# Kernel tuning notes

Hardware: AMD Instinct MI355X
Metric: run time of the kernel (lower is better)

The kernel has to match this reference:

```python
import jax, jax.numpy as jnp
import numpy as np

N = 50000          # nodes
E = 1600000        # edges (avg degree 32)
G = 16             # graphs in batch
H = 128            # hidden_dim
HOP = 3
IN_DIM = 1


def setup_inputs() -> dict:
    key = jax.random.key(0)
    ks = jax.random.split(key, 12)
    s = 1.0 / np.sqrt(H)
    return {
        "x": jax.random.normal(ks[0], (N, IN_DIM), jnp.float32),
        "edge_index": jax.random.randint(ks[1], (2, E), 0, N, jnp.int64),
        "edge_attr": jax.random.uniform(ks[2], (E, 1), jnp.float32),
        "batch": jnp.sort(jax.random.randint(ks[3], (N,), 0, G, jnp.int64)),
        "W1": jax.random.normal(ks[4], (HOP, H, IN_DIM), jnp.float32) * s,
        "W2": jax.random.normal(ks[5], (HOP, H, H), jnp.float32) * s,
        "W3": jax.random.normal(ks[6], (HOP, H, H), jnp.float32) * s,
        "W4": jax.random.normal(ks[7], (HOP, H, 1), jnp.float32) * s,
        "W5": jax.random.normal(ks[8], (1, 2 * H), jnp.float32) * s,
        "b5": jnp.zeros((1,), jnp.float32),
        "W6": jax.random.normal(ks[9], (H, H), jnp.float32) * s,
        "W7": jax.random.normal(ks[10], (H, H), jnp.float32) * s,
    }


def reference(x, edge_index, edge_attr, batch, W1, W2, W3, W4, W5, b5, W6, W7):
    row, col = edge_index[0], edge_index[1]
    node_emb = jnp.zeros((N, H), x.dtype)
    for l in range(HOP):
        nfe = x @ W1[l].T                                        # [N,H]
        # gather neighbor embeddings along col, scatter-add to row
        ne_aggr = jax.ops.segment_sum(node_emb[col], row, num_segments=N)
        efe = jax.nn.relu(edge_attr @ W4[l].T)                   # [E,H]
        ee_aggr = jax.ops.segment_sum(efe, row, num_segments=N)  # [N,H]
        node_emb = jax.nn.relu(nfe + ne_aggr @ W2[l].T + ee_aggr @ W3[l].T)
    pooled = jax.ops.segment_sum(node_emb, batch, num_segments=G)  # [G,H]
    sum_emb = pooled @ W6.T                                        # [G,H]
    cat = jax.nn.relu(jnp.concatenate([sum_emb[batch], node_emb @ W7.T], axis=-1))
    return cat @ W5.T + b5                                         # [N,1]
```

## Files before the change

### kernel.cpp

```cpp
#include <hip/hip_runtime.h>
#include <hip/hip_bf16.h>

#define N_NODES 50000
#define N_EDGES 1600000
#define NGRAPH  16
#define HID     128

#define RPB   128
#define NB    ((N_NODES + RPB - 1) / RPB)
#define NBLK  256
#define EPB   ((N_EDGES + NBLK - 1) / NBLK)
#define P4CAP 6144

typedef unsigned int uint32;
typedef unsigned short ushort;
typedef unsigned char uchar;
typedef __attribute__((ext_vector_type(8))) short bf16x8;
typedef __attribute__((ext_vector_type(4))) float f32x4;
typedef __attribute__((ext_vector_type(2))) float f32x2;

__device__ __forceinline__ uint32 bf16r(float f) {
    uint32 b = __float_as_uint(f);
    return (b + 0x7fffu + ((b >> 16) & 1u)) >> 16;
}
__device__ __forceinline__ uint32 pack_bf16(float lo, float hi) {
    return bf16r(lo) | (bf16r(hi) << 16);
}

__global__ __launch_bounds__(256) void k_init(float* __restrict__ zp, int nz,
                                              const float* __restrict__ W2,
                                              const float* __restrict__ W7,
                                              const float* __restrict__ W3,
                                              const float* __restrict__ W4,
                                              ushort* __restrict__ wpack,
                                              float* __restrict__ v3) {
    int idx = blockIdx.x * 256 + threadIdx.x;
    if (idx < nz) zp[idx] = 0.f;
    if (idx < 4 * 16384) {
        int m = idx >> 14, f = idx & 16383;
        int j = f & 7, lane = (f >> 3) & 63, kk = (f >> 9) & 3, t = (f >> 11) & 7;
        int hp = t * 16 + (lane & 15);
        int k  = kk * 32 + ((lane >> 4) & 3) * 8 + j;
        const float* src = (m < 3) ? (W2 + m * HID * HID) : W7;
        wpack[idx] = (ushort)bf16r(src[hp * HID + k]);
    }
    if (idx < 3 * HID) {
        int l = idx / HID, hp = idx % HID;
        float acc = 0.f;
        for (int h = 0; h < HID; h++)
            acc += W3[l * HID * HID + hp * HID + h] * fmaxf(W4[l * HID + h], 0.f);
        v3[idx] = acc;
    }
}

__global__ __launch_bounds__(1024) void k_p1_hist(const int* __restrict__ row,
                                                  int* __restrict__ blkhist) {
    __shared__ int hist[NB];
    int tid = threadIdx.x, blk = blockIdx.x;
    for (int i = tid; i < NB; i += 1024) hist[i] = 0;
    __syncthreads();
    int s = blk * EPB, e = s + EPB; if (e > N_EDGES) e = N_EDGES;
    for (int i = s + tid; i < e; i += 1024)
        atomicAdd(&hist[row[i] >> 7], 1);
    __syncthreads();
    for (int i = tid; i < NB; i += 1024)
        blkhist[i * NBLK + blk] = hist[i];
}

__global__ __launch_bounds__(NBLK) void k_p2a(int* __restrict__ blkhist,
                                              int* __restrict__ btot) {
    __shared__ int sums[NBLK];
    int t = threadIdx.x, b = blockIdx.x;
    int v = blkhist[b * NBLK + t];
    sums[t] = v;
    __syncthreads();
    for (int d = 1; d < NBLK; d <<= 1) {
        int u = (t >= d) ? sums[t - d] : 0;
        __syncthreads();
        sums[t] += u;
        __syncthreads();
    }
    blkhist[b * NBLK + t] = sums[t] - v;
    if (t == NBLK - 1) btot[b] = sums[t];
}

__global__ __launch_bounds__(1024) void k_p3_part(const int* __restrict__ row,
                                                  const int* __restrict__ col,
                                                  const float* __restrict__ ea,
                                                  const int* __restrict__ blkhist,
                                                  const int* __restrict__ btot,
                                                  int2* __restrict__ pea) {
    __shared__ int sc[512];
    __shared__ int cur[NB];
    int tid = threadIdx.x, blk = blockIdx.x;
    if (tid < 512) sc[tid] = (tid < NB) ? btot[tid] : 0;
    __syncthreads();
    for (int d = 1; d < 512; d <<= 1) {
        int v = 0;
        if (tid < 512 && tid >= d) v = sc[tid - d];
        __syncthreads();
        if (tid < 512) sc[tid] += v;
        __syncthreads();
    }
    for (int i = tid; i < NB; i += 1024)
        cur[i] = (sc[i] - btot[i]) + blkhist[i * NBLK + blk];
    __syncthreads();
    int s = blk * EPB, e = s + EPB; if (e > N_EDGES) e = N_EDGES;
    for (int i = s + tid; i < e; i += 1024) {
        int r = row[i], c = col[i];
        float a = ea[i];
        int slot = atomicAdd(&cur[r >> 7], 1);
        pea[slot] = make_int2(((r & (RPB - 1)) << 16) | c, __float_as_int(a));
    }
}

__global__ __launch_bounds__(512) void k_p4(const int2* __restrict__ pea,
                                            const int* __restrict__ btot,
                                            const float* __restrict__ x,
                                            int* __restrict__ offs,
                                            float* __restrict__ ea_sum,
                                            int* __restrict__ csr,
                                            uchar* __restrict__ emb0,
                                            const float* __restrict__ w1l0,
                                            const float* __restrict__ v3l0) {
    __shared__ int2  cache[P4CAP];
    __shared__ int   red[512];
    __shared__ int   cnt[RPB];
    __shared__ float eas[RPB];
    __shared__ int   scan_s[RPB];
    __shared__ int   curp[RPB];
    int t = threadIdx.x, b = blockIdx.x;
    red[t] = (t < b) ? btot[t] : 0;
    __syncthreads();
    for (int d = 256; d > 0; d >>= 1) {
        if (t < d) red[t] += red[t + d];
        __syncthreads();
    }
    int s = red[0];
    int e = s + btot[b];
    int len = e - s;
    int clen = len < P4CAP ? len : P4CAP;
    for (int i = t; i < clen; i += 512) cache[i] = pea[s + i];
    if (t < RPB) { cnt[t] = 0; eas[t] = 0.f; }
    __syncthreads();
    for (int i = t; i < len; i += 512) {
        int2 p = (i < P4CAP) ? cache[i] : pea[s + i];
        int lr = ((uint32)p.x) >> 16;
        atomicAdd(&cnt[lr], 1);
        atomicAdd(&eas[lr], __int_as_float(p.y));
    }
    __syncthreads();
    if (t < RPB) scan_s[t] = cnt[t];
    __syncthreads();
    for (int d = 1; d < RPB; d <<= 1) {
        int v = 0;
        if (t < RPB && t >= d) v = scan_s[t - d];
        __syncthreads();
        if (t < RPB) scan_s[t] += v;
        __syncthreads();
    }
    int nbase = b * RPB;
    if (t < RPB) {
        int excl = scan_s[t] - cnt[t];
        int n = nbase + t;
        if (n < N_NODES) {
            offs[n] = s + excl;
            ea_sum[n] = eas[t];
        }
        curp[t] = s + excl;
    }
    if (b == NB - 1 && t == 0) offs[N_NODES] = e;
    __syncthreads();
    for (int i = t; i < len; i += 512) {
        int2 p = (i < P4CAP) ? cache[i] : pea[s + i];
        int slot = atomicAdd(&curp[((uint32)p.x) >> 16], 1);
        csr[slot] = p.x & 0xFFFF;
    }
    for (int i = t; i < RPB * 32; i += 512) {
        int lr = i >> 5, c4 = (i & 31) * 4;
        int n = nbase + lr;
        if (n < N_NODES) {
            float xv = x[n];
            float ev = eas[lr];
            float v0 = fmaxf(xv * w1l0[c4 + 0] + ev * v3l0[c4 + 0], 0.f) * 0.015625f;
            float v1 = fmaxf(xv * w1l0[c4 + 1] + ev * v3l0[c4 + 1], 0.f) * 0.015625f;
            float v2 = fmaxf(xv * w1l0[c4 + 2] + ev * v3l0[c4 + 2], 0.f) * 0.015625f;
            float v3v = fmaxf(xv * w1l0[c4 + 3] + ev * v3l0[c4 + 3], 0.f) * 0.015625f;
            int u = __builtin_amdgcn_cvt_pk_fp8_f32(v0, v1, 0, false);
            u = __builtin_amdgcn_cvt_pk_fp8_f32(v2, v3v, u, true);
            *(uint32*)(emb0 + (size_t)n * 128 + c4) = (uint32)u;
        }
    }
}

__global__ __launch_bounds__(256) void k_gather(const uchar* __restrict__ emb,
                                                const int* __restrict__ offs,
                                                const int* __restrict__ csr,
                                                uint32* __restrict__ agg) {
    int node = (blockIdx.x * 256 + threadIdx.x) >> 6;
    int lane = threadIdx.x & 63;
    if (node >= N_NODES) return;
    int s = offs[node], e = offs[node + 1];
    int off2 = 2 * lane;
    float ax[8] = {0.f}, ay[8] = {0.f};
    for (int base = s; base < e; base += 64) {
        int idx = base + lane;
        int cv = (idx < e) ? csr[idx] : 0;
        int cnt = e - base; if (cnt > 64) cnt = 64;
        int j = 0;
        for (; j + 16 <= cnt; j += 16) {
            int h16[16];
#pragma unroll
            for (int u = 0; u < 16; u++) {
                uint32 c = (uint32)__builtin_amdgcn_readlane(cv, j + u);
                h16[u] = *(const ushort*)(emb + (((size_t)c) << 7) + off2);
            }
#pragma unroll
            for (int u = 0; u < 16; u++) {
                f32x2 d = __builtin_amdgcn_cvt_pk_f32_fp8(h16[u], false);
                ax[u & 7] += d.x; ay[u & 7] += d.y;
            }
        }
        for (; j + 4 <= cnt; j += 4) {
            int h4[4];
#pragma unroll
            for (int u = 0; u < 4; u++) {
                uint32 c = (uint32)__builtin_amdgcn_readlane(cv, j + u);
                h4[u] = *(const ushort*)(emb + (((size_t)c) << 7) + off2);
            }
#pragma unroll
            for (int u = 0; u < 4; u++) {
                f32x2 d = __builtin_amdgcn_cvt_pk_f32_fp8(h4[u], false);
                ax[u] += d.x; ay[u] += d.y;
            }
        }
        for (; j < cnt; j++) {
            uint32 c = (uint32)__builtin_amdgcn_readlane(cv, j);
            int h = *(const ushort*)(emb + (((size_t)c) << 7) + off2);
            f32x2 d = __builtin_amdgcn_cvt_pk_f32_fp8(h, false);
            ax[0] += d.x; ay[0] += d.y;
        }
    }
    float rx = (((ax[0] + ax[1]) + (ax[2] + ax[3])) + ((ax[4] + ax[5]) + (ax[6] + ax[7]))) * 64.f;
    float ry = (((ay[0] + ay[1]) + (ay[2] + ay[3])) + ((ay[4] + ay[5]) + (ay[6] + ay[7]))) * 64.f;
    agg[(size_t)node * 64 + lane] = pack_bf16(rx, ry);
}

#define LROW 136

template <bool LAST>
__global__ __launch_bounds__(256) void k_gemm(const uint32* __restrict__ agg,
                                              const ushort* __restrict__ w2p,
                                              const float* __restrict__ w1l,
                                              const float* __restrict__ v3l,
                                              const float* __restrict__ x,
                                              const float* __restrict__ ea_sum,
                                              uchar* __restrict__ emb8Out,
                                              const ushort* __restrict__ w7p,
                                              const float* __restrict__ W5,
                                              float* __restrict__ outp,
                                              const int* __restrict__ batch,
                                              float* __restrict__ pooled) {
    __shared__ ushort tile[64 * LROW];
    __shared__ float redp[4][128];
    int tid = threadIdx.x;
    int tbase = blockIdx.x * 64;
    int wv = tid >> 6, lane = tid & 63;
    int n0 = lane & 15, quad = lane >> 4;
    int arow = wv * 16 + n0;
    bf16x8 a0 = {0,0,0,0,0,0,0,0}, a1 = a0, a2 = a0, a3 = a0;
    if (tbase + arow < N_NODES) {
        const bf16x8* ap = (const bf16x8*)(agg + (size_t)(tbase + arow) * 64);
        a0 = ap[0 + quad]; a1 = ap[4 + quad]; a2 = ap[8 + quad]; a3 = ap[12 + quad];
    }
    const bf16x8* wb = (const bf16x8*)w2p;
    f32x4 acc[8];
#pragma unroll
    for (int t = 0; t < 8; t++) {
        f32x4 c = {0.f, 0.f, 0.f, 0.f};
        c = __builtin_amdgcn_mfma_f32_16x16x32_bf16(a0, wb[(t * 4 + 0) * 64 + lane], c, 0, 0, 0);
        c = __builtin_amdgcn_mfma_f32_16x16x32_bf16(a1, wb[(t * 4 + 1) * 64 + lane], c, 0, 0, 0);
        c = __builtin_amdgcn_mfma_f32_16x16x32_bf16(a2, wb[(t * 4 + 2) * 64 + lane], c, 0, 0, 0);
        c = __builtin_amdgcn_mfma_f32_16x16x32_bf16(a3, wb[(t * 4 + 3) * 64 + lane], c, 0, 0, 0);
        acc[t] = c;
    }
    float xs[4], es[4];
#pragma unroll
    for (int r = 0; r < 4; r++) {
        int n = tbase + wv * 16 + quad * 4 + r;
        xs[r] = (n < N_NODES) ? x[n] : 0.f;
        es[r] = (n < N_NODES) ? ea_sum[n] : 0.f;
    }
    if (!LAST) {
        uchar* stile = (uchar*)tile;
#pragma unroll
        for (int t = 0; t < 8; t++) {
            int hp = t * 16 + n0;
            float w1v = w1l[hp], v3v = v3l[hp];
#pragma unroll
            for (int r = 0; r < 4; r++) {
                float v = fmaxf(acc[t][r] + xs[r] * w1v + es[r] * v3v, 0.f) * 0.015625f;
                int enc = __builtin_amdgcn_cvt_pk_fp8_f32(v, v, 0, false);
                stile[(wv * 16 + quad * 4 + r) * 136 + hp] = (uchar)(enc & 0xff);
            }
        }
        __syncthreads();
        int vn = N_NODES - tbase; if (vn > 64) vn = 64;
        for (int i = tid; i < 64 * 32; i += 256) {
            int r = i >> 5, c4 = (i & 31) * 4;
            if (r < vn) {
                uint32 u = *(const uint32*)&stile[r * 136 + c4];
                *(uint32*)(emb8Out + (size_t)(tbase + r) * 128 + c4) = u;
            }
        }
    } else {
        int nlast = tbase + 63; if (nlast > N_NODES - 1) nlast = N_NODES - 1;
        int g0 = batch[tbase];
        bool uni = (batch[nlast] == g0);
        int gr[4];
        if (!uni) {
#pragma unroll
            for (int r = 0; r < 4; r++) {
                int n = tbase + wv * 16 + quad * 4 + r;
                gr[r] = (n < N_NODES) ? batch[n] : 0;
            }
        }
        float st[8];
#pragma unroll
        for (int t = 0; t < 8; t++) {
            int hp = t * 16 + n0;
            float w1v = w1l[hp], v3v = v3l[hp];
            float stt = 0.f;
#pragma unroll
            for (int r = 0; r < 4; r++) {
                float v = fmaxf(acc[t][r] + xs[r] * w1v + es[r] * v3v, 0.f);
                tile[(wv * 16 + quad * 4 + r) * LROW + hp] = (ushort)bf16r(v);
                if (uni) {
                    stt += v;
                } else {
                    int n = tbase + wv * 16 + quad * 4 + r;
                    if (n < N_NODES) atomicAdd(&pooled[gr[r] * HID + hp], v);
                }
            }
            st[t] = stt;
        }
        if (uni) {
#pragma unroll
            for (int t = 0; t < 8; t++) {
                float v = st[t];
                v += __shfl_xor(v, 16);
                v += __shfl_xor(v, 32);
                if (lane < 16) redp[wv][t * 16 + lane] = v;
            }
        }
        __syncthreads();
        if (uni && tid < 128) {
            float sp = (redp[0][tid] + redp[1][tid]) + (redp[2][tid] + redp[3][tid]);
            atomicAdd(&pooled[g0 * HID + tid], sp);
        }
        bf16x8 b0 = *(const bf16x8*)&tile[arow * LROW + 0 * 32 + quad * 8];
        bf16x8 b1 = *(const bf16x8*)&tile[arow * LROW + 1 * 32 + quad * 8];
        bf16x8 b2 = *(const bf16x8*)&tile[arow * LROW + 2 * 32 + quad * 8];
        bf16x8 b3 = *(const bf16x8*)&tile[arow * LROW + 3 * 32 + quad * 8];
        const bf16x8* w7 = (const bf16x8*)w7p;
        float p[4] = {0.f, 0.f, 0.f, 0.f};
#pragma unroll
        for (int t = 0; t < 8; t++) {
            f32x4 c = {0.f, 0.f, 0.f, 0.f};
            c = __builtin_amdgcn_mfma_f32_16x16x32_bf16(b0, w7[(t * 4 + 0) * 64 + lane], c, 0, 0, 0);
            c = __builtin_amdgcn_mfma_f32_16x16x32_bf16(b1, w7[(t * 4 + 1) * 64 + lane], c, 0, 0, 0);
            c = __builtin_amdgcn_mfma_f32_16x16x32_bf16(b2, w7[(t * 4 + 2) * 64 + lane], c, 0, 0, 0);
            c = __builtin_amdgcn_mfma_f32_16x16x32_bf16(b3, w7[(t * 4 + 3) * 64 + lane], c, 0, 0, 0);
            float w5v = W5[128 + t * 16 + n0];
#pragma unroll
            for (int r = 0; r < 4; r++) p[r] += fmaxf(c[r], 0.f) * w5v;
        }
#pragma unroll
        for (int r = 0; r < 4; r++) {
            float v = p[r];
            v += __shfl_xor(v, 1);
            v += __shfl_xor(v, 2);
            v += __shfl_xor(v, 4);
            v += __shfl_xor(v, 8);
            int n = tbase + wv * 16 + quad * 4 + r;
            if (n0 == 0 && n < N_NODES) outp[n] = v;
        }
    }
}

__global__ __launch_bounds__(256) void k_tail(float* __restrict__ out,
                                              const int* __restrict__ batch,
                                              const float* __restrict__ pooled,
                                              const float* __restrict__ W6,
                                              const float* __restrict__ W5,
                                              const float* __restrict__ b5) {
    __shared__ float red[256];
    __shared__ int gsh[2];
    int t = threadIdx.x;
    int nbase = blockIdx.x * 256;
    int n = nbase + t;
    if (t == 0) gsh[0] = batch[nbase < N_NODES ? nbase : N_NODES - 1];
    if (t == 1) gsh[1] = batch[(nbase + 255) < N_NODES ? (nbase + 255) : N_NODES - 1];
    __syncthreads();
    int g_lo = gsh[0], g_hi = gsh[1];
    int hp = t & 127;
    int g = (t >> 7) ? g_hi : g_lo;
    const float* pg = pooled + g * HID;
    const float* wr = W6 + hp * HID;
    float acc = 0.f;
    for (int h = 0; h < HID; h++) acc += pg[h] * wr[h];
    red[t] = fmaxf(acc, 0.f) * W5[hp];
    __syncthreads();
    for (int d = 64; d > 0; d >>= 1) {
        if (hp < d) red[t] += red[t + d];
        __syncthreads();
    }
    float s_lo = red[0], s_hi = red[128];
    if (n < N_NODES) {
        int gn = batch[n];
        float s;
        if (gn == g_lo) s = s_lo;
        else if (gn == g_hi) s = s_hi;
        else {
            s = 0.f;
            const float* pg2 = pooled + gn * HID;
            for (int hp2 = 0; hp2 < HID; hp2++) {
                float a2 = 0.f;
                for (int h = 0; h < HID; h++) a2 += pg2[h] * W6[hp2 * HID + h];
                s += fmaxf(a2, 0.f) * W5[hp2];
            }
        }
        out[n] += s + b5[0];
    }
}

extern "C" void kernel_launch(void* const* d_in, const int* in_sizes, int n_in,
                              void* d_out, int out_size, void* d_ws, size_t ws_size,
                              hipStream_t stream) {
    (void)in_sizes; (void)n_in; (void)out_size; (void)ws_size;
    const float* x    = (const float*)d_in[0];
    const int*   ei   = (const int*)d_in[1];
    const float* ea   = (const float*)d_in[2];
    const int*   bat  = (const int*)d_in[3];
    const float* W1   = (const float*)d_in[4];
    const float* W2   = (const float*)d_in[5];
    const float* W3   = (const float*)d_in[6];
    const float* W4   = (const float*)d_in[7];
    const float* W5   = (const float*)d_in[8];
    const float* b5   = (const float*)d_in[9];
    const float* W6   = (const float*)d_in[10];
    const float* W7   = (const float*)d_in[11];
    float* out = (float*)d_out;

    const int* row = ei;
    const int* col = ei + N_EDGES;

    float* wsf = (float*)d_ws;
    int*   wsi = (int*)d_ws;
    size_t o = 0;
    float* pooled = wsf + o; o += NGRAPH * HID;
    size_t ztot = o;
    int*   offs   = wsi + o; o += N_NODES + 1;
    float* ea_sum = wsf + o; o += N_NODES;
    int*   btot   = wsi + o; o += NB;
    float* v3     = wsf + o; o += 3 * HID;
    int*   blkh   = wsi + o; o += NB * NBLK;
    o = (o + 3) & ~(size_t)3;
    ushort* wpack = (ushort*)(wsi + o); o += 4 * 16384 / 2;
    int*    csr   = wsi + o; o += N_EDGES;
    o = (o + 1) & ~(size_t)1;
    int2*   pea   = (int2*)(wsi + o); o += 2 * (size_t)N_EDGES;
    uint32* aggB  = (uint32*)(wsi + o); o += (size_t)N_NODES * 64;
    uchar*  emb8  = (uchar*)(wsi + o);  o += (size_t)N_NODES * 32;
    uchar*  emb0  = (uchar*)(wsi + o);  o += (size_t)N_NODES * 32;

    const ushort* w2p1 = wpack + 1 * 16384;
    const ushort* w2p2 = wpack + 2 * 16384;
    const ushort* w7p  = wpack + 3 * 16384;

    k_init<<<(4 * 16384 + 255) / 256, 256, 0, stream>>>(
        (float*)d_ws, (int)ztot, W2, W7, W3, W4, (ushort*)wpack, v3);
    k_p1_hist<<<NBLK, 1024, 0, stream>>>(row, blkh);
    k_p2a<<<NB, NBLK, 0, stream>>>(blkh, btot);
    k_p3_part<<<NBLK, 1024, 0, stream>>>(row, col, ea, blkh, btot, pea);
    k_p4<<<NB, 512, 0, stream>>>(pea, btot, x, offs, ea_sum, csr, emb0, W1, v3);
    k_gather<<<(N_NODES * 64 + 255) / 256, 256, 0, stream>>>(emb0, offs, csr, aggB);
    k_gemm<false><<<(N_NODES + 63) / 64, 256, 0, stream>>>(
        aggB, w2p1, W1 + 1 * HID, v3 + 1 * HID, x, ea_sum, emb8, nullptr, nullptr, nullptr,
        nullptr, nullptr);
    k_gather<<<(N_NODES * 64 + 255) / 256, 256, 0, stream>>>(emb8, offs, csr, aggB);
    k_gemm<true><<<(N_NODES + 63) / 64, 256, 0, stream>>>(
        aggB, w2p2, W1 + 2 * HID, v3 + 2 * HID, x, ea_sum, nullptr, w7p, W5, out, bat, pooled);
    k_tail<<<(N_NODES + 255) / 256, 256, 0, stream>>>(out, bat, pooled, W6, W5, b5);
}
```

Baseline: 259.7 us.

## Fuse neighbor gather into per-hop GEMM kernel via shared-memory tile

The separate gather kernel and GEMM kernel are merged into one k_hop kernel. Each wave aggregates 16 nodes sequentially into a bf16 LDS tile, which the MFMA GEMM then reads directly. This removes the aggB global round trip and two kernel launches, and the next node's CSR indices are prefetched while the current one is processed. In exchange, parallelism per node drops from one wave per node to one wave per 16 nodes processed serially, which can lower memory-level parallelism for the latency-bound gather.

```diff
diff --git a/kernel.cpp b/kernel.cpp
--- a/kernel.cpp
+++ b/kernel.cpp
@@ -193,86 +193,104 @@
     }
 }
 
-__global__ __launch_bounds__(256) void k_gather(const uchar* __restrict__ emb,
-                                                const int* __restrict__ offs,
-                                                const int* __restrict__ csr,
-                                                uint32* __restrict__ agg) {
-    int node = (blockIdx.x * 256 + threadIdx.x) >> 6;
-    int lane = threadIdx.x & 63;
-    if (node >= N_NODES) return;
-    int s = offs[node], e = offs[node + 1];
-    int off2 = 2 * lane;
-    float ax[8] = {0.f}, ay[8] = {0.f};
-    for (int base = s; base < e; base += 64) {
-        int idx = base + lane;
-        int cv = (idx < e) ? csr[idx] : 0;
-        int cnt = e - base; if (cnt > 64) cnt = 64;
-        int j = 0;
-        for (; j + 16 <= cnt; j += 16) {
-            int h16[16];
-#pragma unroll
-            for (int u = 0; u < 16; u++) {
-                uint32 c = (uint32)__builtin_amdgcn_readlane(cv, j + u);
-                h16[u] = *(const ushort*)(emb + (((size_t)c) << 7) + off2);
-            }
-#pragma unroll
-            for (int u = 0; u < 16; u++) {
-                f32x2 d = __builtin_amdgcn_cvt_pk_f32_fp8(h16[u], false);
-                ax[u & 7] += d.x; ay[u & 7] += d.y;
-            }
-        }
-        for (; j + 4 <= cnt; j += 4) {
-            int h4[4];
-#pragma unroll
-            for (int u = 0; u < 4; u++) {
-                uint32 c = (uint32)__builtin_amdgcn_readlane(cv, j + u);
-                h4[u] = *(const ushort*)(emb + (((size_t)c) << 7) + off2);
-            }
-#pragma unroll
-            for (int u = 0; u < 4; u++) {
-                f32x2 d = __builtin_amdgcn_cvt_pk_f32_fp8(h4[u], false);
-                ax[u] += d.x; ay[u] += d.y;
-            }
-        }
-        for (; j < cnt; j++) {
-            uint32 c = (uint32)__builtin_amdgcn_readlane(cv, j);
-            int h = *(const ushort*)(emb + (((size_t)c) << 7) + off2);
-            f32x2 d = __builtin_amdgcn_cvt_pk_f32_fp8(h, false);
-            ax[0] += d.x; ay[0] += d.y;
-        }
-    }
-    float rx = (((ax[0] + ax[1]) + (ax[2] + ax[3])) + ((ax[4] + ax[5]) + (ax[6] + ax[7]))) * 64.f;
-    float ry = (((ay[0] + ay[1]) + (ay[2] + ay[3])) + ((ay[4] + ay[5]) + (ay[6] + ay[7]))) * 64.f;
-    agg[(size_t)node * 64 + lane] = pack_bf16(rx, ry);
-}
-
 #define LROW 136
 
 template <bool LAST>
-__global__ __launch_bounds__(256) void k_gemm(const uint32* __restrict__ agg,
-                                              const ushort* __restrict__ w2p,
-                                              const float* __restrict__ w1l,
-                                              const float* __restrict__ v3l,
-                                              const float* __restrict__ x,
-                                              const float* __restrict__ ea_sum,
-                                              uchar* __restrict__ emb8Out,
-                                              const ushort* __restrict__ w7p,
-                                              const float* __restrict__ W5,
-                                              float* __restrict__ outp,
-                                              const int* __restrict__ batch,
-                                              float* __restrict__ pooled) {
+__global__ __launch_bounds__(256) void k_hop(const uchar* __restrict__ emb,
+                                             const int* __restrict__ offs,
+                                             const int* __restrict__ csr,
+                                             const ushort* __restrict__ w2p,
+                                             const float* __restrict__ w1l,
+                                             const float* __restrict__ v3l,
+                                             const float* __restrict__ x,
+                                             const float* __restrict__ ea_sum,
+                                             uchar* __restrict__ emb8Out,
+                                             const ushort* __restrict__ w7p,
+                                             const float* __restrict__ W5,
+                                             float* __restrict__ outp,
+                                             const int* __restrict__ batch,
+                                             float* __restrict__ pooled) {
     __shared__ ushort tile[64 * LROW];
     __shared__ float redp[4][128];
     int tid = threadIdx.x;
     int tbase = blockIdx.x * 64;
     int wv = tid >> 6, lane = tid & 63;
+    int off2 = 2 * lane;
+    int rbase = tbase + wv * 16;
+
+    {
+        int oi = rbase + lane;
+        int oo = (lane < 17) ? offs[oi <= N_NODES ? oi : N_NODES] : 0;
+        int s0 = __builtin_amdgcn_readlane(oo, 0);
+        int e0 = __builtin_amdgcn_readlane(oo, 1);
+        int cv = (s0 + lane < e0) ? csr[s0 + lane] : 0;
+#pragma unroll 1
+        for (int r = 0; r < 16; r++) {
+            int s = s0, e = e0;
+            int sN = 0, eN = 0, cvN = 0;
+            if (r < 15) {
+                sN = __builtin_amdgcn_readlane(oo, r + 1);
+                eN = __builtin_amdgcn_readlane(oo, r + 2);
+                cvN = (sN + lane < eN) ? csr[sN + lane] : 0;
+            }
+            float ax[8] = {0.f}, ay[8] = {0.f};
+            auto ACC = [&](int cvc, int cnt) {
+                int j = 0;
+                for (; j + 16 <= cnt; j += 16) {
+                    int h16[16];
+#pragma unroll
+                    for (int u = 0; u < 16; u++) {
+                        uint32 c = (uint32)__builtin_amdgcn_readlane(cvc, j + u);
+                        h16[u] = *(const ushort*)(emb + (((size_t)c) << 7) + off2);
+                    }
+#pragma unroll
+                    for (int u = 0; u < 16; u++) {
+                        f32x2 d = __builtin_amdgcn_cvt_pk_f32_fp8(h16[u], false);
+                        ax[u & 7] += d.x; ay[u & 7] += d.y;
+                    }
+                }
+                for (; j + 4 <= cnt; j += 4) {
+                    int h4[4];
+#pragma unroll
+                    for (int u = 0; u < 4; u++) {
+                        uint32 c = (uint32)__builtin_amdgcn_readlane(cvc, j + u);
+                        h4[u] = *(const ushort*)(emb + (((size_t)c) << 7) + off2);
+                    }
+#pragma unroll
+                    for (int u = 0; u < 4; u++) {
+                        f32x2 d = __builtin_amdgcn_cvt_pk_f32_fp8(h4[u], false);
+                        ax[u] += d.x; ay[u] += d.y;
+                    }
+                }
+                for (; j < cnt; j++) {
+                    uint32 c = (uint32)__builtin_amdgcn_readlane(cvc, j);
+                    int h = *(const ushort*)(emb + (((size_t)c) << 7) + off2);
+                    f32x2 d = __builtin_amdgcn_cvt_pk_f32_fp8(h, false);
+                    ax[0] += d.x; ay[0] += d.y;
+                }
+            };
+            int cnt0 = e - s; if (cnt0 > 64) cnt0 = 64;
+            if (cnt0 > 0) ACC(cv, cnt0);
+#pragma unroll 1
+            for (int base = s + 64; base < e; base += 64) {
+                int idx = base + lane;
+                int cvc = (idx < e) ? csr[idx] : 0;
+                int cnt = e - base; if (cnt > 64) cnt = 64;
+                ACC(cvc, cnt);
+            }
+            float rx = (((ax[0] + ax[1]) + (ax[2] + ax[3])) + ((ax[4] + ax[5]) + (ax[6] + ax[7]))) * 64.f;
+            float ry = (((ay[0] + ay[1]) + (ay[2] + ay[3])) + ((ay[4] + ay[5]) + (ay[6] + ay[7]))) * 64.f;
+            *(uint32*)&tile[(wv * 16 + r) * LROW + off2] = pack_bf16(rx, ry);
+            s0 = sN; e0 = eN; cv = cvN;
+        }
+    }
+
     int n0 = lane & 15, quad = lane >> 4;
     int arow = wv * 16 + n0;
-    bf16x8 a0 = {0,0,0,0,0,0,0,0}, a1 = a0, a2 = a0, a3 = a0;
-    if (tbase + arow < N_NODES) {
-        const bf16x8* ap = (const bf16x8*)(agg + (size_t)(tbase + arow) * 64);
-        a0 = ap[0 + quad]; a1 = ap[4 + quad]; a2 = ap[8 + quad]; a3 = ap[12 + quad];
-    }
+    bf16x8 a0 = *(const bf16x8*)&tile[arow * LROW + 0 * 32 + quad * 8];
+    bf16x8 a1 = *(const bf16x8*)&tile[arow * LROW + 1 * 32 + quad * 8];
+    bf16x8 a2 = *(const bf16x8*)&tile[arow * LROW + 2 * 32 + quad * 8];
+    bf16x8 a3 = *(const bf16x8*)&tile[arow * LROW + 3 * 32 + quad * 8];
     const bf16x8* wb = (const bf16x8*)w2p;
     f32x4 acc[8];
 #pragma unroll
@@ -292,6 +310,7 @@
         es[r] = (n < N_NODES) ? ea_sum[n] : 0.f;
     }
     if (!LAST) {
+        __syncthreads();
         uchar* stile = (uchar*)tile;
 #pragma unroll
         for (int t = 0; t < 8; t++) {
@@ -470,7 +489,6 @@
     int*    csr   = wsi + o; o += N_EDGES;
     o = (o + 1) & ~(size_t)1;
     int2*   pea   = (int2*)(wsi + o); o += 2 * (size_t)N_EDGES;
-    uint32* aggB  = (uint32*)(wsi + o); o += (size_t)N_NODES * 64;
     uchar*  emb8  = (uchar*)(wsi + o);  o += (size_t)N_NODES * 32;
     uchar*  emb0  = (uchar*)(wsi + o);  o += (size_t)N_NODES * 32;
 
@@ -484,12 +502,11 @@
     k_p2a<<<NB, NBLK, 0, stream>>>(blkh, btot);
     k_p3_part<<<NBLK, 1024, 0, stream>>>(row, col, ea, blkh, btot, pea);
     k_p4<<<NB, 512, 0, stream>>>(pea, btot, x, offs, ea_sum, csr, emb0, W1, v3);
-    k_gather<<<(N_NODES * 64 + 255) / 256, 256, 0, stream>>>(emb0, offs, csr, aggB);
-    k_gemm<false><<<(N_NODES + 63) / 64, 256, 0, stream>>>(
-        aggB, w2p1, W1 + 1 * HID, v3 + 1 * HID, x, ea_sum, emb8, nullptr, nullptr, nullptr,
-        nullptr, nullptr);
-    k_gather<<<(N_NODES * 64 + 255) / 256, 256, 0, stream>>>(emb8, offs, csr, aggB);
-    k_gemm<true><<<(N_NODES + 63) / 64, 256, 0, stream>>>(
-        aggB, w2p2, W1 + 2 * HID, v3 + 2 * HID, x, ea_sum, nullptr, w7p, W5, out, bat, pooled);
+    k_hop<false><<<(N_NODES + 63) / 64, 256, 0, stream>>>(
+        emb0, offs, csr, w2p1, W1 + 1 * HID, v3 + 1 * HID, x, ea_sum, emb8,
+        nullptr, nullptr, nullptr, nullptr, nullptr);
+    k_hop<true><<<(N_NODES + 63) / 64, 256, 0, stream>>>(
+        emb8, offs, csr, w2p2, W1 + 2 * HID, v3 + 2 * HID, x, ea_sum, nullptr,
+        w7p, W5, out, bat, pooled);
     k_tail<<<(N_NODES + 255) / 256, 256, 0, stream>>>(out, bat, pooled, W6, W5, b5);
 }
```

After: 267.9 us. 1.03x slower.
